# Kernel tuning notes

Hardware: AMD Instinct MI355X
Metric: run time of the kernel (lower is better)

Reference implementation:

```python
import jax, jax.numpy as jnp
import numpy as np

def setup_inputs() -> dict:
    key = jax.random.key(0)
    k1, k2, k3, k4, k5 = jax.random.split(key, 5)
    vocab, embed, hidden = 32000, 1024, 1024
    batch, src_len = 64, 512
    src = jax.random.randint(k1, (batch, src_len), 0, vocab)
    emb_table = jax.random.normal(k2, (vocab, embed), dtype=jnp.float32)
    # xavier_uniform bounds
    bx = float(np.sqrt(6.0 / (embed + hidden)))
    bh = float(np.sqrt(6.0 / (hidden + hidden)))
    W_xh = jax.random.uniform(k3, (hidden, embed), minval=-bx, maxval=bx, dtype=jnp.float32)
    b_xh = jax.random.uniform(k4, (hidden,), minval=-1.0/np.sqrt(embed), maxval=1.0/np.sqrt(embed), dtype=jnp.float32)
    W_hh = jax.random.uniform(k5, (hidden, hidden), minval=-bh, maxval=bh, dtype=jnp.float32)
    return {"src": src, "emb_table": emb_table, "W_xh": W_xh, "b_xh": b_xh, "W_hh": W_hh}

def reference(src, emb_table, W_xh, b_xh, W_hh):
    # embedded: (batch, src_len, embed)
    embedded = emb_table[src]
    # precompute input projection for all timesteps: (batch, src_len, hidden)
    x_proj = jnp.einsum('bte,he->bth', embedded, W_xh) + b_xh
    batch = src.shape[0]
    hidden = W_hh.shape[0]
    h0 = jnp.zeros((batch, hidden), dtype=jnp.float32)

    def step(h, x_t):
        h_new = jnp.tanh(x_t + h @ W_hh.T)
        return h_new, None

    # scan over time: x_proj transposed to (src_len, batch, hidden)
    h_final, _ = jax.lax.scan(step, h0, jnp.swapaxes(x_proj, 0, 1))
    return h_final
```

## Files before the change

### kernel.cpp

```cpp
#include <hip/hip_runtime.h>
#include <hip/hip_fp16.h>

typedef _Float16 half8 __attribute__((ext_vector_type(8)));
typedef float floatx4 __attribute__((ext_vector_type(4)));

#define HBUF_BYTES (2ull * 16 * 1024 * 8)
#define CTL_BYTES  (32ull * 1024)
#define XP_OFF     (HBUF_BYTES + CTL_BYTES)
#define XP_BYTES   (512ull * 64 * 1024 * 2)
#define FLAG_STRIDE 16

union pack4 { unsigned long long u; _Float16 h[4]; };

__device__ inline half8 cvt8(const float4 a, const float4 b) {
    half8 r;
    r[0] = (_Float16)a.x; r[1] = (_Float16)a.y; r[2] = (_Float16)a.z; r[3] = (_Float16)a.w;
    r[4] = (_Float16)b.x; r[5] = (_Float16)b.y; r[6] = (_Float16)b.z; r[7] = (_Float16)b.w;
    return r;
}

__global__ __launch_bounds__(256) void xproj_kernel(
    const int* __restrict__ src, const float* __restrict__ emb,
    const float* __restrict__ Wxh, const float* __restrict__ bxh,
    _Float16* __restrict__ xp)
{
    __shared__ _Float16 As[128][40];
    __shared__ _Float16 Bs[128][40];

    const int tid  = threadIdx.x;
    const int lane = tid & 63;
    const int w    = tid >> 6;
    const int m15  = lane & 15;
    const int quad = lane >> 4;
    const int bid  = blockIdx.x;
    const int bn   = bid & 7;
    const int bm   = bid >> 3;
    const int m0   = bm * 128, n0 = bn * 128;
    const int wm   = w & 1, wn = w >> 1;

    const int  srow = tid >> 1;
    const int  scol = (tid & 1) * 16;
    const long arow = (long)src[m0 + srow] * 1024;
    const float* abase = emb + arow + scol;
    const float* bbase = Wxh + (long)(n0 + srow) * 1024 + scol;

    floatx4 zero4 = {0.f, 0.f, 0.f, 0.f};
    floatx4 acc[4][4];
#pragma unroll
    for (int mt = 0; mt < 4; mt++)
#pragma unroll
        for (int nt = 0; nt < 4; nt++) acc[mt][nt] = zero4;

    for (int k0 = 0; k0 < 1024; k0 += 32) {
        __syncthreads();
        float4 a0 = *(const float4*)(abase + k0);
        float4 a1 = *(const float4*)(abase + k0 + 4);
        float4 a2 = *(const float4*)(abase + k0 + 8);
        float4 a3 = *(const float4*)(abase + k0 + 12);
        float4 b0 = *(const float4*)(bbase + k0);
        float4 b1 = *(const float4*)(bbase + k0 + 4);
        float4 b2 = *(const float4*)(bbase + k0 + 8);
        float4 b3 = *(const float4*)(bbase + k0 + 12);
        *(half8*)&As[srow][scol]     = cvt8(a0, a1);
        *(half8*)&As[srow][scol + 8] = cvt8(a2, a3);
        *(half8*)&Bs[srow][scol]     = cvt8(b0, b1);
        *(half8*)&Bs[srow][scol + 8] = cvt8(b2, b3);
        __syncthreads();

        half8 af[4], bf[4];
#pragma unroll
        for (int mt = 0; mt < 4; mt++)
            af[mt] = *(const half8*)&As[wm * 64 + mt * 16 + m15][quad * 8];
#pragma unroll
        for (int nt = 0; nt < 4; nt++)
            bf[nt] = *(const half8*)&Bs[wn * 64 + nt * 16 + m15][quad * 8];
#pragma unroll
        for (int mt = 0; mt < 4; mt++)
#pragma unroll
            for (int nt = 0; nt < 4; nt++)
                acc[mt][nt] = __builtin_amdgcn_mfma_f32_16x16x32_f16(
                    af[mt], bf[nt], acc[mt][nt], 0, 0, 0);
    }

#pragma unroll
    for (int nt = 0; nt < 4; nt++) {
        const int n = n0 + wn * 64 + nt * 16 + m15;
        const float bias = bxh[n];
#pragma unroll
        for (int mt = 0; mt < 4; mt++) {
            const int mrow = m0 + wm * 64 + mt * 16 + quad * 4;
#pragma unroll
            for (int r = 0; r < 4; r++) {
                const int m = mrow + r;
                const int b = m >> 9;
                const int t = m & 511;
                xp[((long)t * 64 + b) * 1024 + n] = (_Float16)(acc[mt][nt][r] + bias);
            }
        }
    }
}

__global__ __launch_bounds__(256, 1) void rnn_kernel(
    const float* __restrict__ Whh, const _Float16* __restrict__ xp,
    unsigned long long* __restrict__ hb, int* __restrict__ flags,
    float* __restrict__ out)
{
    __shared__ _Float16 hstage[16][1032];
    __shared__ floatx4  cred[4][4][64];

    const int tid    = threadIdx.x;
    const int lane   = tid & 63;
    const int w      = tid >> 6;
    const int m15    = lane & 15;
    const int quad   = lane >> 4;
    const int wg     = blockIdx.x;
    const int g      = wg & 15;
    const int member = wg >> 4;
    const int b0     = g * 4;

    for (int i = tid; i < 16 * 1032; i += 256) ((_Float16*)hstage)[i] = (_Float16)0.f;

    half8 Wf[4][8];
#pragma unroll
    for (int nt = 0; nt < 4; nt++) {
        const float* wrow = Whh + (long)(member * 64 + nt * 16 + m15) * 1024
                                + w * 256 + quad * 8;
#pragma unroll
        for (int kk = 0; kk < 8; kk++) {
            float4 lo = *(const float4*)(wrow + kk * 32);
            float4 hi = *(const float4*)(wrow + kk * 32 + 4);
            Wf[nt][kk] = cvt8(lo, hi);
        }
    }
    __syncthreads();

    const int dim = member * 64 + w * 16 + m15;
    float xv[4] = {0.f, 0.f, 0.f, 0.f};
    if (quad == 0) {
#pragma unroll
        for (int r = 0; r < 4; r++)
            xv[r] = (float)xp[((long)0 * 64 + b0 + r) * 1024 + dim];
    }

    int* myflag = flags + (g * 16 + member) * FLAG_STRIDE;
    const int* gflags = flags + g * 16 * FLAG_STRIDE;
    floatx4 zero4 = {0.f, 0.f, 0.f, 0.f};

    for (int t = 0; t < 512; t++) {
        if (t > 0) {
            if (tid < 16) {
                const int* fw = gflags + tid * FLAG_STRIDE;
                while (__hip_atomic_load(fw, __ATOMIC_RELAXED,
                                         __HIP_MEMORY_SCOPE_AGENT) < t) { }
            }
            __syncthreads();
        }

        {
            const unsigned long long* hcu =
                hb + (size_t)(t & 1) * 16384 + (size_t)g * 1024 + (size_t)tid * 4;
            uint4 v0, v1;
            asm volatile(
                "global_load_dwordx4 %0, %2, off sc0 sc1\n\t"
                "global_load_dwordx4 %1, %2, off offset:16 sc0 sc1\n\t"
                "s_waitcnt vmcnt(0)"
                : "=&v"(v0), "=&v"(v1)
                : "v"(hcu)
                : "memory");

            unsigned long long u[4];
            u[0] = ((unsigned long long)v0.y << 32) | v0.x;
            u[1] = ((unsigned long long)v0.w << 32) | v0.z;
            u[2] = ((unsigned long long)v1.y << 32) | v1.x;
            u[3] = ((unsigned long long)v1.w << 32) | v1.z;
#pragma unroll
            for (int b = 0; b < 4; b++) {
                unsigned long long q = 0;
#pragma unroll
                for (int e = 0; e < 4; e++)
                    q |= ((u[e] >> (16 * b)) & 0xffffull) << (16 * e);
                *(unsigned long long*)&hstage[b][tid * 4] = q;
            }
        }
        __syncthreads();

        floatx4 pacc[4];
#pragma unroll
        for (int nt = 0; nt < 4; nt++) pacc[nt] = zero4;
#pragma unroll
        for (int kk = 0; kk < 8; kk++) {
            half8 a = *(const half8*)&hstage[m15][w * 256 + kk * 32 + quad * 8];
#pragma unroll
            for (int nt = 0; nt < 4; nt++)
                pacc[nt] = __builtin_amdgcn_mfma_f32_16x16x32_f16(
                    a, Wf[nt][kk], pacc[nt], 0, 0, 0);
        }

#pragma unroll
        for (int nt = 0; nt < 4; nt++) cred[w][nt][lane] = pacc[nt];
        __syncthreads();
        floatx4 dsum = cred[0][w][lane];
#pragma unroll
        for (int ww = 1; ww < 4; ww++) dsum += cred[ww][w][lane];

        if (quad == 0) {
            pack4 p;
#pragma unroll
            for (int r = 0; r < 4; r++) {
                float pre  = dsum[r] + xv[r];
                float e    = __expf(2.0f * pre);
                float hval = 1.0f - 2.0f / (e + 1.0f);
                p.h[r] = (_Float16)hval;
                if (t == 511) out[(b0 + r) * 1024 + dim] = hval;
            }
            unsigned long long* hnu =
                hb + (size_t)((t + 1) & 1) * 16384 + (size_t)g * 1024;
            __hip_atomic_store(hnu + dim, p.u, __ATOMIC_RELAXED,
                               __HIP_MEMORY_SCOPE_AGENT);
        }

        __syncthreads();
        if (tid == 0)
            __hip_atomic_store(myflag, t + 1, __ATOMIC_RELAXED,
                               __HIP_MEMORY_SCOPE_AGENT);

        if (t < 511 && quad == 0) {
#pragma unroll
            for (int r = 0; r < 4; r++)
                xv[r] = (float)xp[((long)(t + 1) * 64 + b0 + r) * 1024 + dim];
        }
    }
}

extern "C" void kernel_launch(void* const* d_in, const int* in_sizes, int n_in,
                              void* d_out, int out_size, void* d_ws, size_t ws_size,
                              hipStream_t stream) {
    const int*   src = (const int*)d_in[0];
    const float* emb = (const float*)d_in[1];
    const float* Wxh = (const float*)d_in[2];
    const float* bxh = (const float*)d_in[3];
    const float* Whh = (const float*)d_in[4];
    float* out = (float*)d_out;

    char* ws = (char*)d_ws;
    unsigned long long* hb = (unsigned long long*)ws;
    int* flags = (int*)(ws + HBUF_BYTES);
    _Float16* xp = (_Float16*)(ws + XP_OFF);

    (void)hipMemsetAsync(ws, 0, HBUF_BYTES + CTL_BYTES, stream);

    hipLaunchKernelGGL(xproj_kernel, dim3(2048), dim3(256), 0, stream,
                       src, emb, Wxh, bxh, xp);

    hipLaunchKernelGGL(rnn_kernel, dim3(256), dim3(256), 0, stream,
                       Whh, xp, hb, flags, out);
}
```

Measured before the change: 1.320 ms.

## Fuse input projection and recurrence into one persistent kernel with per-chunk readiness gating

The input-projection GEMM and the RNN recurrence now run in a single launch. 64 recurrence blocks spin on per-quarter done counters while 2048 projection blocks produce x_proj in time-ordered chunks, so the recurrence can start before the whole projection finishes. The recurrence is also re-partitioned from 256 blocks of 4 batch rows to 64 blocks of 16 batch rows. Each wave now holds its full K slice of W_hh in registers, which removes the cross-wave LDS reduction. The scheme relies on the 64 recurrence blocks being resident while the projection blocks are scheduled, which risks deadlock or contention, and each step now has fewer blocks and a longer serial MFMA chain.

```diff
diff --git a/kernel.cpp b/kernel.cpp
--- a/kernel.cpp
+++ b/kernel.cpp
@@ -4,13 +4,14 @@
 typedef _Float16 half8 __attribute__((ext_vector_type(8)));
 typedef float floatx4 __attribute__((ext_vector_type(4)));
 
-#define HBUF_BYTES (2ull * 16 * 1024 * 8)
+#define HBUF_BYTES (2ull * 4 * 1024 * 4 * 8)
 #define CTL_BYTES  (32ull * 1024)
+#define DONE_OFF_INTS 4096
 #define XP_OFF     (HBUF_BYTES + CTL_BYTES)
-#define XP_BYTES   (512ull * 64 * 1024 * 2)
 #define FLAG_STRIDE 16
 
 union pack4 { unsigned long long u; _Float16 h[4]; };
+union hbits { _Float16 f; unsigned short s; };
 
 __device__ inline half8 cvt8(const float4 a, const float4 b) {
     half8 r;
@@ -19,22 +20,23 @@
     return r;
 }
 
-__global__ __launch_bounds__(256) void xproj_kernel(
-    const int* __restrict__ src, const float* __restrict__ emb,
-    const float* __restrict__ Wxh, const float* __restrict__ bxh,
-    _Float16* __restrict__ xp)
+__device__ void xproj_body(char* smem, int bid2,
+                           const int* __restrict__ src, const float* __restrict__ emb,
+                           const float* __restrict__ Wxh, const float* __restrict__ bxh,
+                           _Float16* __restrict__ xp, int* __restrict__ done)
 {
-    __shared__ _Float16 As[128][40];
-    __shared__ _Float16 Bs[128][40];
+    _Float16 (*As)[40] = reinterpret_cast<_Float16(*)[40]>(smem);
+    _Float16 (*Bs)[40] = reinterpret_cast<_Float16(*)[40]>(smem + 10240);
 
     const int tid  = threadIdx.x;
     const int lane = tid & 63;
     const int w    = tid >> 6;
     const int m15  = lane & 15;
     const int quad = lane >> 4;
-    const int bid  = blockIdx.x;
-    const int bn   = bid & 7;
-    const int bm   = bid >> 3;
+    const int q    = bid2 >> 9;
+    const int jj   = (bid2 >> 3) & 63;
+    const int bn   = bid2 & 7;
+    const int bm   = jj * 4 + q;
     const int m0   = bm * 128, n0 = bn * 128;
     const int wm   = w & 1, wn = w >> 1;
 
@@ -98,15 +100,49 @@
             }
         }
     }
-}
-
-__global__ __launch_bounds__(256, 1) void rnn_kernel(
-    const float* __restrict__ Whh, const _Float16* __restrict__ xp,
-    unsigned long long* __restrict__ hb, int* __restrict__ flags,
-    float* __restrict__ out)
+
+    __syncthreads();
+    if (tid == 0)
+        __hip_atomic_fetch_add(done + q * 16, 1, __ATOMIC_RELEASE,
+                               __HIP_MEMORY_SCOPE_AGENT);
+}
+
+__device__ inline void xp_gate(const int* done, int tn) {
+    if ((tn & 127) == 0) {
+        if (threadIdx.x == 0) {
+            const int* dq = done + (tn >> 7) * 16;
+            while (__hip_atomic_load(dq, __ATOMIC_RELAXED,
+                                     __HIP_MEMORY_SCOPE_AGENT) < 512)
+                __builtin_amdgcn_s_sleep(8);
+        }
+        __syncthreads();
+    }
+}
+
+__device__ inline void xp_load4(const _Float16* p, float* xv) {
+    unsigned r0, r1, r2, r3;
+    asm volatile(
+        "global_load_ushort %0, %4, off sc0 sc1\n\t"
+        "global_load_ushort %1, %4, off offset:2048 sc0 sc1\n\t"
+        "global_load_ushort %2, %5, off sc0 sc1\n\t"
+        "global_load_ushort %3, %5, off offset:2048 sc0 sc1\n\t"
+        "s_waitcnt vmcnt(0)"
+        : "=&v"(r0), "=&v"(r1), "=&v"(r2), "=&v"(r3)
+        : "v"(p), "v"(p + 2048)
+        : "memory");
+    hbits h;
+    h.s = (unsigned short)r0; xv[0] = (float)h.f;
+    h.s = (unsigned short)r1; xv[1] = (float)h.f;
+    h.s = (unsigned short)r2; xv[2] = (float)h.f;
+    h.s = (unsigned short)r3; xv[3] = (float)h.f;
+}
+
+__device__ void rnn_body(char* smem,
+                         const float* __restrict__ Whh, const _Float16* __restrict__ xp,
+                         unsigned long long* __restrict__ hb, int* __restrict__ flags,
+                         const int* __restrict__ done, float* __restrict__ out)
 {
-    __shared__ _Float16 hstage[16][1032];
-    __shared__ floatx4  cred[4][4][64];
+    _Float16 (*hstage)[1032] = reinterpret_cast<_Float16(*)[1032]>(smem);
 
     const int tid    = threadIdx.x;
     const int lane   = tid & 63;
@@ -114,33 +150,24 @@
     const int m15    = lane & 15;
     const int quad   = lane >> 4;
     const int wg     = blockIdx.x;
-    const int g      = wg & 15;
-    const int member = wg >> 4;
-    const int b0     = g * 4;
-
-    for (int i = tid; i < 16 * 1032; i += 256) ((_Float16*)hstage)[i] = (_Float16)0.f;
-
-    half8 Wf[4][8];
-#pragma unroll
-    for (int nt = 0; nt < 4; nt++) {
-        const float* wrow = Whh + (long)(member * 64 + nt * 16 + m15) * 1024
-                                + w * 256 + quad * 8;
-#pragma unroll
-        for (int kk = 0; kk < 8; kk++) {
-            float4 lo = *(const float4*)(wrow + kk * 32);
-            float4 hi = *(const float4*)(wrow + kk * 32 + 4);
-            Wf[nt][kk] = cvt8(lo, hi);
-        }
-    }
-    __syncthreads();
-
-    const int dim = member * 64 + w * 16 + m15;
-    float xv[4] = {0.f, 0.f, 0.f, 0.f};
-    if (quad == 0) {
-#pragma unroll
-        for (int r = 0; r < 4; r++)
-            xv[r] = (float)xp[((long)0 * 64 + b0 + r) * 1024 + dim];
-    }
+    const int g      = wg & 3;
+    const int member = wg >> 2;
+    const int b0     = g * 16;
+    const int dim    = member * 64 + w * 16 + m15;
+    const int myb    = b0 + quad * 4;
+
+    half8 Wf[32];
+#pragma unroll
+    for (int kk = 0; kk < 32; kk++) {
+        const float* wrow = Whh + (long)dim * 1024 + kk * 32 + quad * 8;
+        float4 lo = *(const float4*)(wrow);
+        float4 hi = *(const float4*)(wrow + 4);
+        Wf[kk] = cvt8(lo, hi);
+    }
+
+    float xv[4];
+    xp_gate(done, 0);
+    xp_load4(xp + (size_t)myb * 1024 + dim, xv);
 
     int* myflag = flags + (g * 16 + member) * FLAG_STRIDE;
     const int* gflags = flags + g * 16 * FLAG_STRIDE;
@@ -151,85 +178,106 @@
             if (tid < 16) {
                 const int* fw = gflags + tid * FLAG_STRIDE;
                 while (__hip_atomic_load(fw, __ATOMIC_RELAXED,
-                                         __HIP_MEMORY_SCOPE_AGENT) < t) { }
+                                         __HIP_MEMORY_SCOPE_AGENT) < t)
+                    __builtin_amdgcn_s_sleep(1);
             }
             __syncthreads();
         }
 
         {
-            const unsigned long long* hcu =
-                hb + (size_t)(t & 1) * 16384 + (size_t)g * 1024 + (size_t)tid * 4;
-            uint4 v0, v1;
+            const char* hcu = (const char*)hb
+                + ((size_t)(t & 1) * 4 + g) * 32768 + (size_t)tid * 128;
+            uint4 v0, v1, v2, v3, v4, v5, v6, v7;
             asm volatile(
-                "global_load_dwordx4 %0, %2, off sc0 sc1\n\t"
-                "global_load_dwordx4 %1, %2, off offset:16 sc0 sc1\n\t"
+                "global_load_dwordx4 %0, %8, off sc0 sc1\n\t"
+                "global_load_dwordx4 %1, %8, off offset:16 sc0 sc1\n\t"
+                "global_load_dwordx4 %2, %8, off offset:32 sc0 sc1\n\t"
+                "global_load_dwordx4 %3, %8, off offset:48 sc0 sc1\n\t"
+                "global_load_dwordx4 %4, %8, off offset:64 sc0 sc1\n\t"
+                "global_load_dwordx4 %5, %8, off offset:80 sc0 sc1\n\t"
+                "global_load_dwordx4 %6, %8, off offset:96 sc0 sc1\n\t"
+                "global_load_dwordx4 %7, %8, off offset:112 sc0 sc1\n\t"
                 "s_waitcnt vmcnt(0)"
-                : "=&v"(v0), "=&v"(v1)
+                : "=&v"(v0), "=&v"(v1), "=&v"(v2), "=&v"(v3),
+                  "=&v"(v4), "=&v"(v5), "=&v"(v6), "=&v"(v7)
                 : "v"(hcu)
                 : "memory");
 
-            unsigned long long u[4];
-            u[0] = ((unsigned long long)v0.y << 32) | v0.x;
-            u[1] = ((unsigned long long)v0.w << 32) | v0.z;
-            u[2] = ((unsigned long long)v1.y << 32) | v1.x;
-            u[3] = ((unsigned long long)v1.w << 32) | v1.z;
-#pragma unroll
-            for (int b = 0; b < 4; b++) {
+            unsigned long long u[16];
+            u[0]  = ((unsigned long long)v0.y << 32) | v0.x;
+            u[1]  = ((unsigned long long)v0.w << 32) | v0.z;
+            u[2]  = ((unsigned long long)v1.y << 32) | v1.x;
+            u[3]  = ((unsigned long long)v1.w << 32) | v1.z;
+            u[4]  = ((unsigned long long)v2.y << 32) | v2.x;
+            u[5]  = ((unsigned long long)v2.w << 32) | v2.z;
+            u[6]  = ((unsigned long long)v3.y << 32) | v3.x;
+            u[7]  = ((unsigned long long)v3.w << 32) | v3.z;
+            u[8]  = ((unsigned long long)v4.y << 32) | v4.x;
+            u[9]  = ((unsigned long long)v4.w << 32) | v4.z;
+            u[10] = ((unsigned long long)v5.y << 32) | v5.x;
+            u[11] = ((unsigned long long)v5.w << 32) | v5.z;
+            u[12] = ((unsigned long long)v6.y << 32) | v6.x;
+            u[13] = ((unsigned long long)v6.w << 32) | v6.z;
+            u[14] = ((unsigned long long)v7.y << 32) | v7.x;
+            u[15] = ((unsigned long long)v7.w << 32) | v7.z;
+
+#pragma unroll
+            for (int b = 0; b < 16; b++) {
+                const int j = b >> 2, s = 16 * (b & 3);
                 unsigned long long q = 0;
 #pragma unroll
                 for (int e = 0; e < 4; e++)
-                    q |= ((u[e] >> (16 * b)) & 0xffffull) << (16 * e);
+                    q |= ((u[4 * e + j] >> s) & 0xffffull) << (16 * e);
                 *(unsigned long long*)&hstage[b][tid * 4] = q;
             }
         }
         __syncthreads();
 
-        floatx4 pacc[4];
-#pragma unroll
-        for (int nt = 0; nt < 4; nt++) pacc[nt] = zero4;
-#pragma unroll
-        for (int kk = 0; kk < 8; kk++) {
-            half8 a = *(const half8*)&hstage[m15][w * 256 + kk * 32 + quad * 8];
-#pragma unroll
-            for (int nt = 0; nt < 4; nt++)
-                pacc[nt] = __builtin_amdgcn_mfma_f32_16x16x32_f16(
-                    a, Wf[nt][kk], pacc[nt], 0, 0, 0);
-        }
-
-#pragma unroll
-        for (int nt = 0; nt < 4; nt++) cred[w][nt][lane] = pacc[nt];
-        __syncthreads();
-        floatx4 dsum = cred[0][w][lane];
-#pragma unroll
-        for (int ww = 1; ww < 4; ww++) dsum += cred[ww][w][lane];
-
-        if (quad == 0) {
-            pack4 p;
-#pragma unroll
-            for (int r = 0; r < 4; r++) {
-                float pre  = dsum[r] + xv[r];
-                float e    = __expf(2.0f * pre);
-                float hval = 1.0f - 2.0f / (e + 1.0f);
-                p.h[r] = (_Float16)hval;
-                if (t == 511) out[(b0 + r) * 1024 + dim] = hval;
-            }
-            unsigned long long* hnu =
-                hb + (size_t)((t + 1) & 1) * 16384 + (size_t)g * 1024;
-            __hip_atomic_store(hnu + dim, p.u, __ATOMIC_RELAXED,
-                               __HIP_MEMORY_SCOPE_AGENT);
-        }
+        floatx4 pacc = zero4;
+#pragma unroll
+        for (int kk = 0; kk < 32; kk++) {
+            half8 a = *(const half8*)&hstage[m15][kk * 32 + quad * 8];
+            pacc = __builtin_amdgcn_mfma_f32_16x16x32_f16(a, Wf[kk], pacc, 0, 0, 0);
+        }
+
+        pack4 p;
+#pragma unroll
+        for (int r = 0; r < 4; r++) {
+            float pre  = pacc[r] + xv[r];
+            float e    = __expf(2.0f * pre);
+            float hval = 1.0f - 2.0f / (e + 1.0f);
+            p.h[r] = (_Float16)hval;
+            if (t == 511) out[(size_t)(myb + r) * 1024 + dim] = hval;
+        }
+        __hip_atomic_store(
+            hb + (((size_t)((t + 1) & 1) * 4 + g) * 1024 + dim) * 4 + quad,
+            p.u, __ATOMIC_RELAXED, __HIP_MEMORY_SCOPE_AGENT);
 
         __syncthreads();
         if (tid == 0)
             __hip_atomic_store(myflag, t + 1, __ATOMIC_RELAXED,
                                __HIP_MEMORY_SCOPE_AGENT);
 
-        if (t < 511 && quad == 0) {
-#pragma unroll
-            for (int r = 0; r < 4; r++)
-                xv[r] = (float)xp[((long)(t + 1) * 64 + b0 + r) * 1024 + dim];
-        }
-    }
+        if (t < 511) {
+            xp_gate(done, t + 1);
+            xp_load4(xp + ((size_t)(t + 1) * 64 + myb) * 1024 + dim, xv);
+        }
+    }
+}
+
+__global__ __launch_bounds__(256, 1) void fused_kernel(
+    const int* __restrict__ src, const float* __restrict__ emb,
+    const float* __restrict__ Wxh, const float* __restrict__ bxh,
+    const float* __restrict__ Whh, _Float16* __restrict__ xp,
+    unsigned long long* __restrict__ hb, int* __restrict__ flags,
+    int* __restrict__ done, float* __restrict__ out)
+{
+    __shared__ __align__(16) char smem[33024];
+    if (blockIdx.x >= 64) {
+        xproj_body(smem, blockIdx.x - 64, src, emb, Wxh, bxh, xp, done);
+        return;
+    }
+    rnn_body(smem, Whh, xp, hb, flags, done, out);
 }
 
 extern "C" void kernel_launch(void* const* d_in, const int* in_sizes, int n_in,
@@ -245,13 +293,11 @@
     char* ws = (char*)d_ws;
     unsigned long long* hb = (unsigned long long*)ws;
     int* flags = (int*)(ws + HBUF_BYTES);
+    int* done  = flags + DONE_OFF_INTS;
     _Float16* xp = (_Float16*)(ws + XP_OFF);
 
     (void)hipMemsetAsync(ws, 0, HBUF_BYTES + CTL_BYTES, stream);
 
-    hipLaunchKernelGGL(xproj_kernel, dim3(2048), dim3(256), 0, stream,
-                       src, emb, Wxh, bxh, xp);
-
-    hipLaunchKernelGGL(rnn_kernel, dim3(256), dim3(256), 0, stream,
-                       Whh, xp, hb, flags, out);
-}
+    hipLaunchKernelGGL(fused_kernel, dim3(2112), dim3(256), 0, stream,
+                       src, emb, Wxh, bxh, Whh, xp, hb, flags, done, out);
+}
```

New measurement: 2.009 ms. 1.52x slower.
